# Kernel optimization log

Hardware: AMD Instinct MI355X
Metric: run time of the kernel (lower is better)

The kernel has to match this reference:

```python
import jax, jax.numpy as jnp
import numpy as np

B, L, S, H, E, D = 4, 2048, 2048, 8, 64, 64

def setup_inputs() -> dict:
    key = jax.random.key(0)
    kq, kk, kv = jax.random.split(key, 3)
    queries = jax.random.normal(kq, (B, L, H, E), dtype=jnp.float32)
    keys = jax.random.normal(kk, (B, S, H, E), dtype=jnp.float32)
    values = jax.random.normal(kv, (B, S, H, D), dtype=jnp.float32)
    return {"queries": queries, "keys": keys, "values": values}

def reference(queries, keys, values):
    # scale = self.scale or 1/sqrt(E)
    scale = 1.0 / jnp.sqrt(jnp.float32(queries.shape[-1]))
    # scores: [B, H, L, S]
    scores = jnp.einsum('blhe,bshe->bhls', queries, keys)
    # dropout is identity at inference (Keras Dropout only active in training)
    A = jax.nn.softmax(scale * scores, axis=-1)
    # output: [B, L, H, D]
    return jnp.einsum('bhls,bshd->blhd', A, values)
```

## Files before the change

kernel.cpp:

```cpp
#include <hip/hip_runtime.h>


#define B_ 4
#define L_ 2048
#define S_ 2048
#define H_ 8
#define E_ 64
#define D_ 64

#define NUMSZ (B_ * L_ * H_ * D_)
#define LSZ (B_ * L_ * H_)
#define KVELEM (B_ * H_ * S_ * 64)
#define TILE_ELEMS 2048

typedef __attribute__((ext_vector_type(8))) __bf16 bf16x8;
typedef __attribute__((ext_vector_type(4))) __bf16 bf16x4;
typedef __attribute__((ext_vector_type(16))) float floatx16;

union BF4U { bf16x4 v; uint2 u; };
union BF8U { bf16x8 v; uint4 u; };

__device__ __forceinline__ void async_load16(const void* g, void* l) {
  __builtin_amdgcn_global_load_lds(
      (const __attribute__((address_space(1))) unsigned int*)g,
      (__attribute__((address_space(3))) unsigned int*)l, 16, 0, 0);
}

__device__ __forceinline__ bf16x8 cvt8(float4 a, float4 b) {
  bf16x8 r;
  r[0] = (__bf16)a.x; r[1] = (__bf16)a.y; r[2] = (__bf16)a.z; r[3] = (__bf16)a.w;
  r[4] = (__bf16)b.x; r[5] = (__bf16)b.y; r[6] = (__bf16)b.z; r[7] = (__bf16)b.w;
  return r;
}

__global__ __launch_bounds__(256) void prep_kernel(const float* __restrict__ K,
                                                   const float* __restrict__ V,
                                                   __bf16* __restrict__ Kb,
                                                   __bf16* __restrict__ Vb) {
  __shared__ float Vs[32 * 64];
  const int bid = blockIdx.x;
  const int tile = bid & 63;
  const int h = (bid >> 6) & 7;
  const int b = bid >> 9;
  const int s0 = tile * 32;
  const int i = threadIdx.x;

  {
    const int s = i >> 3, cp = i & 7;
    const int e0 = 8 * (cp ^ (s & 7));
    const float* src = K + (((size_t)(b * S_ + s0 + s) * H_ + h) * E_ + e0);
    float4 a = *(const float4*)src;
    float4 bb = *(const float4*)(src + 4);
    *(bf16x8*)(Kb + (size_t)bid * TILE_ELEMS + i * 8) = cvt8(a, bb);
  }
  {
    const int s = i >> 3, d0 = (i & 7) * 8;
    const float* src = V + (((size_t)(b * S_ + s0 + s) * H_ + h) * D_ + d0);
    float4 a = *(const float4*)src;
    float4 bb = *(const float4*)(src + 4);
    *(float4*)&Vs[s * 64 + d0] = a;
    *(float4*)&Vs[s * 64 + d0 + 4] = bb;
  }
  __syncthreads();
  {
    const int Ll = i >> 3, cp = i & 7;
    const int ci = cp ^ (Ll & 7);
    const int d = 2 * Ll + (ci >> 2);
    const int ch = ci & 3;
    BF8U o;
#pragma unroll
    for (int j = 0; j < 8; ++j) o.v[j] = (__bf16)Vs[(8 * ch + j) * 64 + d];
    *(bf16x8*)(Vb + (size_t)bid * TILE_ELEMS + i * 8) = o.v;
  }
}

__global__ __launch_bounds__(256, 3) void attn_kernel(const float* __restrict__ Q,
                                                      const __bf16* __restrict__ Kb,
                                                      const __bf16* __restrict__ Vb,
                                                      float* __restrict__ O,
                                                      float* __restrict__ num_ws,
                                                      float* __restrict__ l_ws,
                                                      int splits) {
  __shared__ __align__(16) __bf16 Kt[2][2 * TILE_ELEMS];
  __shared__ __align__(16) __bf16 Vt[2][2 * TILE_ELEMS];

  const int tid = threadIdx.x;
  const int lane = tid & 63;
  const int wave = tid >> 6;
  const int q32 = lane & 31;
  const int h32 = lane >> 5;

  const int bid = blockIdx.x;
  const int qb = bid & 15;
  const int h = (bid >> 4) & 7;
  const int b = (bid >> 7) & 3;
  const int split = bid >> 9;

  const int NT2 = (S_ / 32) / splits / 2;
  const int tile0 = split * NT2 * 2;

  const float qscale = 0.125f * 1.44269504088896340736f;
  const int qrow = qb * 128 + wave * 32 + q32;
  const float* qp = Q + ((size_t)(b * L_ + qrow) * H_ + h) * E_;
  bf16x8 qf[4];
#pragma unroll
  for (int c = 0; c < 4; ++c) {
    const float* p = qp + c * 16 + h32 * 8;
    float4 a = *(const float4*)p;
    float4 bb = *(const float4*)(p + 4);
    float t[8] = {a.x, a.y, a.z, a.w, bb.x, bb.y, bb.z, bb.w};
#pragma unroll
    for (int j = 0; j < 8; ++j) qf[c][j] = (__bf16)(t[j] * qscale);
  }

  int koff[4];
#pragma unroll
  for (int c = 0; c < 4; ++c) koff[c] = (q32 * 8 + (((2 * c + h32) ^ (q32 & 7)))) * 8;
  int voff[2][2];
#pragma unroll
  for (int s2 = 0; s2 < 2; ++s2)
#pragma unroll
    for (int dt = 0; dt < 2; ++dt) {
      int dp = dt * 32 + q32;
      int Ll = dp >> 1;
      int ci = (dp & 1) * 4 + 2 * s2 + h32;
      voff[s2][dt] = (Ll * 8 + (ci ^ (Ll & 7))) * 8;
    }

  float l = 0.0f;
  floatx16 ot[2][2];
#pragma unroll
  for (int sb = 0; sb < 2; ++sb)
#pragma unroll
    for (int r = 0; r < 16; ++r) { ot[sb][0][r] = 0.f; ot[sb][1][r] = 0.f; }

  const __bf16* KbBH = Kb + (size_t)((b * H_ + h) * 64) * TILE_ELEMS;
  const __bf16* VbBH = Vb + (size_t)((b * H_ + h) * 64) * TILE_ELEMS;
  const int lin8 = (wave * 64 + lane) * 8;

#pragma unroll
  for (int st = 0; st < 2; ++st) {
    async_load16(KbBH + (size_t)(tile0 + st) * TILE_ELEMS + lin8,
                 &Kt[0][st * TILE_ELEMS + wave * 512]);
    async_load16(VbBH + (size_t)(tile0 + st) * TILE_ELEMS + lin8,
                 &Vt[0][st * TILE_ELEMS + wave * 512]);
  }

  for (int t = 0; t < NT2; ++t) {
    const int buf = t & 1;
    __syncthreads();

    if (t + 1 < NT2) {
#pragma unroll
      for (int st = 0; st < 2; ++st) {
        async_load16(KbBH + (size_t)(tile0 + 2 * (t + 1) + st) * TILE_ELEMS + lin8,
                     &Kt[buf ^ 1][st * TILE_ELEMS + wave * 512]);
        async_load16(VbBH + (size_t)(tile0 + 2 * (t + 1) + st) * TILE_ELEMS + lin8,
                     &Vt[buf ^ 1][st * TILE_ELEMS + wave * 512]);
      }
    }

#pragma unroll
    for (int sb = 0; sb < 2; ++sb) {
      const __bf16* Kbuf = &Kt[buf][sb * TILE_ELEMS];
      const __bf16* Vbuf = &Vt[buf][sb * TILE_ELEMS];

      floatx16 sc;
#pragma unroll
      for (int r = 0; r < 16; ++r) sc[r] = 0.f;
#pragma unroll
      for (int c = 0; c < 4; ++c) {
        bf16x8 kA = *(const bf16x8*)&Kbuf[koff[c]];
        sc = __builtin_amdgcn_mfma_f32_32x32x16_bf16(kA, qf[c], sc, 0, 0, 0);
      }

      BF4U pg[4];
#pragma unroll
      for (int g = 0; g < 4; ++g) {
        float p0 = __builtin_amdgcn_exp2f(sc[4 * g + 0]);
        float p1 = __builtin_amdgcn_exp2f(sc[4 * g + 1]);
        float p2 = __builtin_amdgcn_exp2f(sc[4 * g + 2]);
        float p3 = __builtin_amdgcn_exp2f(sc[4 * g + 3]);
        l += (p0 + p1) + (p2 + p3);
        pg[g].v = (bf16x4){(__bf16)p0, (__bf16)p1, (__bf16)p2, (__bf16)p3};
      }
      uint2 sendA = h32 ? pg[0].u : pg[1].u;
      uint2 sendB = h32 ? pg[2].u : pg[3].u;
      uint2 recvA, recvB;
      recvA.x = __shfl_xor((int)sendA.x, 32);
      recvA.y = __shfl_xor((int)sendA.y, 32);
      recvB.x = __shfl_xor((int)sendB.x, 32);
      recvB.y = __shfl_xor((int)sendB.y, 32);
      BF8U pB0, pB1;
      if (h32 == 0) {
        pB0.u = (uint4){pg[0].u.x, pg[0].u.y, recvA.x, recvA.y};
        pB1.u = (uint4){pg[2].u.x, pg[2].u.y, recvB.x, recvB.y};
      } else {
        pB0.u = (uint4){recvA.x, recvA.y, pg[1].u.x, pg[1].u.y};
        pB1.u = (uint4){recvB.x, recvB.y, pg[3].u.x, pg[3].u.y};
      }

      bf16x8 vA00 = *(const bf16x8*)&Vbuf[voff[0][0]];
      bf16x8 vA01 = *(const bf16x8*)&Vbuf[voff[0][1]];
      bf16x8 vA10 = *(const bf16x8*)&Vbuf[voff[1][0]];
      bf16x8 vA11 = *(const bf16x8*)&Vbuf[voff[1][1]];
      ot[sb][0] = __builtin_amdgcn_mfma_f32_32x32x16_bf16(vA00, pB0.v, ot[sb][0], 0, 0, 0);
      ot[sb][1] = __builtin_amdgcn_mfma_f32_32x32x16_bf16(vA01, pB0.v, ot[sb][1], 0, 0, 0);
      ot[sb][0] = __builtin_amdgcn_mfma_f32_32x32x16_bf16(vA10, pB1.v, ot[sb][0], 0, 0, 0);
      ot[sb][1] = __builtin_amdgcn_mfma_f32_32x32x16_bf16(vA11, pB1.v, ot[sb][1], 0, 0, 0);
    }
  }

  l += __shfl_xor(l, 32);
  floatx16 om[2];
#pragma unroll
  for (int dt = 0; dt < 2; ++dt)
#pragma unroll
    for (int r = 0; r < 16; ++r) om[dt][r] = ot[0][dt][r] + ot[1][dt][r];

  if (splits == 1) {
    const float inv = 1.0f / l;
    float* orow = O + ((size_t)(b * L_ + qrow) * H_ + h) * D_;
#pragma unroll
    for (int dt = 0; dt < 2; ++dt)
#pragma unroll
      for (int g = 0; g < 4; ++g) {
        float4 v = {om[dt][4 * g + 0] * inv, om[dt][4 * g + 1] * inv,
                    om[dt][4 * g + 2] * inv, om[dt][4 * g + 3] * inv};
        *(float4*)(orow + dt * 32 + g * 8 + h32 * 4) = v;
      }
  } else {
    float* nrow = num_ws + (size_t)split * NUMSZ + ((size_t)(b * L_ + qrow) * H_ + h) * D_;
#pragma unroll
    for (int dt = 0; dt < 2; ++dt)
#pragma unroll
      for (int g = 0; g < 4; ++g) {
        float4 v = {om[dt][4 * g + 0], om[dt][4 * g + 1], om[dt][4 * g + 2],
                    om[dt][4 * g + 3]};
        *(float4*)(nrow + dt * 32 + g * 8 + h32 * 4) = v;
      }
    if (h32 == 0) l_ws[(size_t)split * LSZ + (size_t)(b * L_ + qrow) * H_ + h] = l;
  }
}

__global__ __launch_bounds__(256) void combine_kernel(const float* __restrict__ num_ws,
                                                      const float* __restrict__ l_ws,
                                                      float* __restrict__ O, int splits) {
  const size_t i4 = ((size_t)blockIdx.x * 256 + threadIdx.x) * 4;
  float4 acc = {0.f, 0.f, 0.f, 0.f};
  float lt = 0.f;
  for (int s = 0; s < splits; ++s) {
    float4 v = *(const float4*)(num_ws + (size_t)s * NUMSZ + i4);
    acc.x += v.x; acc.y += v.y; acc.z += v.z; acc.w += v.w;
    lt += l_ws[(size_t)s * LSZ + (i4 >> 6)];
  }
  const float inv = 1.0f / lt;
  float4 o = {acc.x * inv, acc.y * inv, acc.z * inv, acc.w * inv};
  *(float4*)(O + i4) = o;
}

extern "C" void kernel_launch(void* const* d_in, const int* in_sizes, int n_in,
                              void* d_out, int out_size, void* d_ws, size_t ws_size,
                              hipStream_t stream) {
  const float* Q = (const float*)d_in[0];
  const float* K = (const float*)d_in[1];
  const float* V = (const float*)d_in[2];
  float* O = (float*)d_out;

  __bf16* Kb = (__bf16*)d_ws;
  __bf16* Vb = Kb + KVELEM;
  float* num_ws = (float*)(Vb + KVELEM);
  const size_t base = (size_t)2 * KVELEM * sizeof(__bf16);
  const size_t per_split = ((size_t)NUMSZ + (size_t)LSZ) * sizeof(float);
  int splits = 1;
  if (ws_size >= base + 4 * per_split) splits = 4;
  else if (ws_size >= base + 2 * per_split) splits = 2;
  float* l_ws = num_ws + (size_t)splits * NUMSZ;

  prep_kernel<<<B_ * H_ * 64, 256, 0, stream>>>(K, V, Kb, Vb);
  dim3 grid(B_ * H_ * (L_ / 128) * splits);
  attn_kernel<<<grid, 256, 0, stream>>>(Q, Kb, Vb, O, num_ws, l_ws, splits);
  if (splits > 1) {
    combine_kernel<<<NUMSZ / 4 / 256, 256, 0, stream>>>(num_ws, l_ws, O, splits);
  }
}
```

Baseline: 154.8 us.

## Process two 32-row query groups per wave to reuse K/V fragments

Each wave now handles 64 query rows (two 32-row groups) instead of 32, so every K and V fragment read from LDS feeds two MFMA chains. The query block grows to 256 rows, the grid halves, and the split-K count is capped at 2 instead of 4. The goal is fewer LDS reads and less global K/V traffic per unit of work. In exchange, register pressure rises (launch bounds drop to 2 blocks per CU) and fewer blocks are launched, which may hurt occupancy and latency hiding.

```diff
diff --git a/kernel.cpp b/kernel.cpp
--- a/kernel.cpp
+++ b/kernel.cpp
@@ -5,10 +5,8 @@
 #define L_ 2048
 #define S_ 2048
 #define H_ 8
-#define E_ 64
-#define D_ 64
-
-#define NUMSZ (B_ * L_ * H_ * D_)
+
+#define NUMSZ (B_ * L_ * H_ * 64)
 #define LSZ (B_ * L_ * H_)
 #define KVELEM (B_ * H_ * S_ * 64)
 #define TILE_ELEMS 2048
@@ -31,6 +29,37 @@
   r[0] = (__bf16)a.x; r[1] = (__bf16)a.y; r[2] = (__bf16)a.z; r[3] = (__bf16)a.w;
   r[4] = (__bf16)b.x; r[5] = (__bf16)b.y; r[6] = (__bf16)b.z; r[7] = (__bf16)b.w;
   return r;
+}
+
+__device__ __forceinline__ void softmax_pb(const floatx16& sc, int h32, float& l,
+                                           bf16x8& pB0v, bf16x8& pB1v) {
+  BF4U pg[4];
+#pragma unroll
+  for (int g = 0; g < 4; ++g) {
+    float p0 = __builtin_amdgcn_exp2f(sc[4 * g + 0]);
+    float p1 = __builtin_amdgcn_exp2f(sc[4 * g + 1]);
+    float p2 = __builtin_amdgcn_exp2f(sc[4 * g + 2]);
+    float p3 = __builtin_amdgcn_exp2f(sc[4 * g + 3]);
+    l += (p0 + p1) + (p2 + p3);
+    pg[g].v = (bf16x4){(__bf16)p0, (__bf16)p1, (__bf16)p2, (__bf16)p3};
+  }
+  uint2 sendA = h32 ? pg[0].u : pg[1].u;
+  uint2 sendB = h32 ? pg[2].u : pg[3].u;
+  uint2 recvA, recvB;
+  recvA.x = __shfl_xor((int)sendA.x, 32);
+  recvA.y = __shfl_xor((int)sendA.y, 32);
+  recvB.x = __shfl_xor((int)sendB.x, 32);
+  recvB.y = __shfl_xor((int)sendB.y, 32);
+  BF8U pB0, pB1;
+  if (h32 == 0) {
+    pB0.u = (uint4){pg[0].u.x, pg[0].u.y, recvA.x, recvA.y};
+    pB1.u = (uint4){pg[2].u.x, pg[2].u.y, recvB.x, recvB.y};
+  } else {
+    pB0.u = (uint4){recvA.x, recvA.y, pg[1].u.x, pg[1].u.y};
+    pB1.u = (uint4){recvB.x, recvB.y, pg[3].u.x, pg[3].u.y};
+  }
+  pB0v = pB0.v;
+  pB1v = pB1.v;
 }
 
 __global__ __launch_bounds__(256) void prep_kernel(const float* __restrict__ K,
@@ -48,14 +77,14 @@
   {
     const int s = i >> 3, cp = i & 7;
     const int e0 = 8 * (cp ^ (s & 7));
-    const float* src = K + (((size_t)(b * S_ + s0 + s) * H_ + h) * E_ + e0);
+    const float* src = K + (((size_t)(b * S_ + s0 + s) * H_ + h) * 64 + e0);
     float4 a = *(const float4*)src;
     float4 bb = *(const float4*)(src + 4);
     *(bf16x8*)(Kb + (size_t)bid * TILE_ELEMS + i * 8) = cvt8(a, bb);
   }
   {
     const int s = i >> 3, d0 = (i & 7) * 8;
-    const float* src = V + (((size_t)(b * S_ + s0 + s) * H_ + h) * D_ + d0);
+    const float* src = V + (((size_t)(b * S_ + s0 + s) * H_ + h) * 64 + d0);
     float4 a = *(const float4*)src;
     float4 bb = *(const float4*)(src + 4);
     *(float4*)&Vs[s * 64 + d0] = a;
@@ -74,7 +103,7 @@
   }
 }
 
-__global__ __launch_bounds__(256, 3) void attn_kernel(const float* __restrict__ Q,
+__global__ __launch_bounds__(256, 2) void attn_kernel(const float* __restrict__ Q,
                                                       const __bf16* __restrict__ Kb,
                                                       const __bf16* __restrict__ Vb,
                                                       float* __restrict__ O,
@@ -91,26 +120,29 @@
   const int h32 = lane >> 5;
 
   const int bid = blockIdx.x;
-  const int qb = bid & 15;
-  const int h = (bid >> 4) & 7;
-  const int b = (bid >> 7) & 3;
-  const int split = bid >> 9;
+  const int qb = bid & 7;
+  const int h = (bid >> 3) & 7;
+  const int b = (bid >> 6) & 3;
+  const int split = bid >> 8;
 
   const int NT2 = (S_ / 32) / splits / 2;
   const int tile0 = split * NT2 * 2;
 
   const float qscale = 0.125f * 1.44269504088896340736f;
-  const int qrow = qb * 128 + wave * 32 + q32;
-  const float* qp = Q + ((size_t)(b * L_ + qrow) * H_ + h) * E_;
-  bf16x8 qf[4];
-#pragma unroll
-  for (int c = 0; c < 4; ++c) {
-    const float* p = qp + c * 16 + h32 * 8;
-    float4 a = *(const float4*)p;
-    float4 bb = *(const float4*)(p + 4);
-    float t[8] = {a.x, a.y, a.z, a.w, bb.x, bb.y, bb.z, bb.w};
-#pragma unroll
-    for (int j = 0; j < 8; ++j) qf[c][j] = (__bf16)(t[j] * qscale);
+  const int qrow0 = qb * 256 + wave * 64 + q32;
+  bf16x8 qf[2][4];
+#pragma unroll
+  for (int g = 0; g < 2; ++g) {
+    const float* qp = Q + ((size_t)(b * L_ + qrow0 + g * 32) * H_ + h) * 64;
+#pragma unroll
+    for (int c = 0; c < 4; ++c) {
+      const float* p = qp + c * 16 + h32 * 8;
+      float4 a = *(const float4*)p;
+      float4 bb = *(const float4*)(p + 4);
+      float t[8] = {a.x, a.y, a.z, a.w, bb.x, bb.y, bb.z, bb.w};
+#pragma unroll
+      for (int j = 0; j < 8; ++j) qf[g][c][j] = (__bf16)(t[j] * qscale);
+    }
   }
 
   int koff[4];
@@ -127,12 +159,12 @@
       voff[s2][dt] = (Ll * 8 + (ci ^ (Ll & 7))) * 8;
     }
 
-  float l = 0.0f;
+  float l[2] = {0.f, 0.f};
   floatx16 ot[2][2];
 #pragma unroll
-  for (int sb = 0; sb < 2; ++sb)
-#pragma unroll
-    for (int r = 0; r < 16; ++r) { ot[sb][0][r] = 0.f; ot[sb][1][r] = 0.f; }
+  for (int g = 0; g < 2; ++g)
+#pragma unroll
+    for (int r = 0; r < 16; ++r) { ot[g][0][r] = 0.f; ot[g][1][r] = 0.f; }
 
   const __bf16* KbBH = Kb + (size_t)((b * H_ + h) * 64) * TILE_ELEMS;
   const __bf16* VbBH = Vb + (size_t)((b * H_ + h) * 64) * TILE_ELEMS;
@@ -165,81 +197,69 @@
       const __bf16* Kbuf = &Kt[buf][sb * TILE_ELEMS];
       const __bf16* Vbuf = &Vt[buf][sb * TILE_ELEMS];
 
-      floatx16 sc;
-#pragma unroll
-      for (int r = 0; r < 16; ++r) sc[r] = 0.f;
-#pragma unroll
-      for (int c = 0; c < 4; ++c) {
-        bf16x8 kA = *(const bf16x8*)&Kbuf[koff[c]];
-        sc = __builtin_amdgcn_mfma_f32_32x32x16_bf16(kA, qf[c], sc, 0, 0, 0);
-      }
-
-      BF4U pg[4];
-#pragma unroll
-      for (int g = 0; g < 4; ++g) {
-        float p0 = __builtin_amdgcn_exp2f(sc[4 * g + 0]);
-        float p1 = __builtin_amdgcn_exp2f(sc[4 * g + 1]);
-        float p2 = __builtin_amdgcn_exp2f(sc[4 * g + 2]);
-        float p3 = __builtin_amdgcn_exp2f(sc[4 * g + 3]);
-        l += (p0 + p1) + (p2 + p3);
-        pg[g].v = (bf16x4){(__bf16)p0, (__bf16)p1, (__bf16)p2, (__bf16)p3};
-      }
-      uint2 sendA = h32 ? pg[0].u : pg[1].u;
-      uint2 sendB = h32 ? pg[2].u : pg[3].u;
-      uint2 recvA, recvB;
-      recvA.x = __shfl_xor((int)sendA.x, 32);
-      recvA.y = __shfl_xor((int)sendA.y, 32);
-      recvB.x = __shfl_xor((int)sendB.x, 32);
-      recvB.y = __shfl_xor((int)sendB.y, 32);
-      BF8U pB0, pB1;
-      if (h32 == 0) {
-        pB0.u = (uint4){pg[0].u.x, pg[0].u.y, recvA.x, recvA.y};
-        pB1.u = (uint4){pg[2].u.x, pg[2].u.y, recvB.x, recvB.y};
-      } else {
-        pB0.u = (uint4){recvA.x, recvA.y, pg[1].u.x, pg[1].u.y};
-        pB1.u = (uint4){recvB.x, recvB.y, pg[3].u.x, pg[3].u.y};
-      }
-
-      bf16x8 vA00 = *(const bf16x8*)&Vbuf[voff[0][0]];
-      bf16x8 vA01 = *(const bf16x8*)&Vbuf[voff[0][1]];
-      bf16x8 vA10 = *(const bf16x8*)&Vbuf[voff[1][0]];
-      bf16x8 vA11 = *(const bf16x8*)&Vbuf[voff[1][1]];
-      ot[sb][0] = __builtin_amdgcn_mfma_f32_32x32x16_bf16(vA00, pB0.v, ot[sb][0], 0, 0, 0);
-      ot[sb][1] = __builtin_amdgcn_mfma_f32_32x32x16_bf16(vA01, pB0.v, ot[sb][1], 0, 0, 0);
-      ot[sb][0] = __builtin_amdgcn_mfma_f32_32x32x16_bf16(vA10, pB1.v, ot[sb][0], 0, 0, 0);
-      ot[sb][1] = __builtin_amdgcn_mfma_f32_32x32x16_bf16(vA11, pB1.v, ot[sb][1], 0, 0, 0);
-    }
-  }
-
-  l += __shfl_xor(l, 32);
-  floatx16 om[2];
-#pragma unroll
-  for (int dt = 0; dt < 2; ++dt)
-#pragma unroll
-    for (int r = 0; r < 16; ++r) om[dt][r] = ot[0][dt][r] + ot[1][dt][r];
-
-  if (splits == 1) {
-    const float inv = 1.0f / l;
-    float* orow = O + ((size_t)(b * L_ + qrow) * H_ + h) * D_;
-#pragma unroll
-    for (int dt = 0; dt < 2; ++dt)
-#pragma unroll
-      for (int g = 0; g < 4; ++g) {
-        float4 v = {om[dt][4 * g + 0] * inv, om[dt][4 * g + 1] * inv,
-                    om[dt][4 * g + 2] * inv, om[dt][4 * g + 3] * inv};
-        *(float4*)(orow + dt * 32 + g * 8 + h32 * 4) = v;
-      }
-  } else {
-    float* nrow = num_ws + (size_t)split * NUMSZ + ((size_t)(b * L_ + qrow) * H_ + h) * D_;
-#pragma unroll
-    for (int dt = 0; dt < 2; ++dt)
-#pragma unroll
-      for (int g = 0; g < 4; ++g) {
-        float4 v = {om[dt][4 * g + 0], om[dt][4 * g + 1], om[dt][4 * g + 2],
-                    om[dt][4 * g + 3]};
-        *(float4*)(nrow + dt * 32 + g * 8 + h32 * 4) = v;
-      }
-    if (h32 == 0) l_ws[(size_t)split * LSZ + (size_t)(b * L_ + qrow) * H_ + h] = l;
+      bf16x8 kA[4];
+#pragma unroll
+      for (int c = 0; c < 4; ++c) kA[c] = *(const bf16x8*)&Kbuf[koff[c]];
+
+      floatx16 sc0, sc1;
+#pragma unroll
+      for (int r = 0; r < 16; ++r) { sc0[r] = 0.f; sc1[r] = 0.f; }
+#pragma unroll
+      for (int c = 0; c < 4; ++c)
+        sc0 = __builtin_amdgcn_mfma_f32_32x32x16_bf16(kA[c], qf[0][c], sc0, 0, 0, 0);
+#pragma unroll
+      for (int c = 0; c < 4; ++c)
+        sc1 = __builtin_amdgcn_mfma_f32_32x32x16_bf16(kA[c], qf[1][c], sc1, 0, 0, 0);
+
+      bf16x8 p00, p01, p10, p11;
+      softmax_pb(sc0, h32, l[0], p00, p01);
+      softmax_pb(sc1, h32, l[1], p10, p11);
+
+      bf16x8 vA[4];
+      vA[0] = *(const bf16x8*)&Vbuf[voff[0][0]];
+      vA[1] = *(const bf16x8*)&Vbuf[voff[0][1]];
+      vA[2] = *(const bf16x8*)&Vbuf[voff[1][0]];
+      vA[3] = *(const bf16x8*)&Vbuf[voff[1][1]];
+      ot[0][0] = __builtin_amdgcn_mfma_f32_32x32x16_bf16(vA[0], p00, ot[0][0], 0, 0, 0);
+      ot[0][1] = __builtin_amdgcn_mfma_f32_32x32x16_bf16(vA[1], p00, ot[0][1], 0, 0, 0);
+      ot[1][0] = __builtin_amdgcn_mfma_f32_32x32x16_bf16(vA[0], p10, ot[1][0], 0, 0, 0);
+      ot[1][1] = __builtin_amdgcn_mfma_f32_32x32x16_bf16(vA[1], p10, ot[1][1], 0, 0, 0);
+      ot[0][0] = __builtin_amdgcn_mfma_f32_32x32x16_bf16(vA[2], p01, ot[0][0], 0, 0, 0);
+      ot[0][1] = __builtin_amdgcn_mfma_f32_32x32x16_bf16(vA[3], p01, ot[0][1], 0, 0, 0);
+      ot[1][0] = __builtin_amdgcn_mfma_f32_32x32x16_bf16(vA[2], p11, ot[1][0], 0, 0, 0);
+      ot[1][1] = __builtin_amdgcn_mfma_f32_32x32x16_bf16(vA[3], p11, ot[1][1], 0, 0, 0);
+    }
+  }
+
+#pragma unroll
+  for (int g = 0; g < 2; ++g) {
+    float lg = l[g] + __shfl_xor(l[g], 32);
+    const int qrow = qrow0 + g * 32;
+    if (splits == 1) {
+      const float inv = 1.0f / lg;
+      float* orow = O + ((size_t)(b * L_ + qrow) * H_ + h) * 64;
+#pragma unroll
+      for (int dt = 0; dt < 2; ++dt)
+#pragma unroll
+        for (int gg = 0; gg < 4; ++gg) {
+          float4 v = {ot[g][dt][4 * gg + 0] * inv, ot[g][dt][4 * gg + 1] * inv,
+                      ot[g][dt][4 * gg + 2] * inv, ot[g][dt][4 * gg + 3] * inv};
+          *(float4*)(orow + dt * 32 + gg * 8 + h32 * 4) = v;
+        }
+    } else {
+      float* nrow =
+          num_ws + (size_t)split * NUMSZ + ((size_t)(b * L_ + qrow) * H_ + h) * 64;
+#pragma unroll
+      for (int dt = 0; dt < 2; ++dt)
+#pragma unroll
+        for (int gg = 0; gg < 4; ++gg) {
+          float4 v = {ot[g][dt][4 * gg + 0], ot[g][dt][4 * gg + 1],
+                      ot[g][dt][4 * gg + 2], ot[g][dt][4 * gg + 3]};
+          *(float4*)(nrow + dt * 32 + gg * 8 + h32 * 4) = v;
+        }
+      if (h32 == 0)
+        l_ws[(size_t)split * LSZ + (size_t)(b * L_ + qrow) * H_ + h] = lg;
+    }
   }
 }
 
@@ -273,12 +293,11 @@
   const size_t base = (size_t)2 * KVELEM * sizeof(__bf16);
   const size_t per_split = ((size_t)NUMSZ + (size_t)LSZ) * sizeof(float);
   int splits = 1;
-  if (ws_size >= base + 4 * per_split) splits = 4;
-  else if (ws_size >= base + 2 * per_split) splits = 2;
+  if (ws_size >= base + 2 * per_split) splits = 2;
   float* l_ws = num_ws + (size_t)splits * NUMSZ;
 
   prep_kernel<<<B_ * H_ * 64, 256, 0, stream>>>(K, V, Kb, Vb);
-  dim3 grid(B_ * H_ * (L_ / 128) * splits);
+  dim3 grid(B_ * H_ * (L_ / 256) * splits);
   attn_kernel<<<grid, 256, 0, stream>>>(Q, Kb, Vb, O, num_ws, l_ws, splits);
   if (splits > 1) {
     combine_kernel<<<NUMSZ / 4 / 256, 256, 0, stream>>>(num_ws, l_ws, O, splits);
```

Measured after the change: 145.4 us. 6.1% less time.
